# Kernel optimization log

Measured on AMD Instinct MI355X. Metric: run time of the kernel, lower is better.

## Reference

```python
import jax, jax.numpy as jnp
import numpy as np

DIM = 256
HEADS = 8
WH, WW = 8, 8
N = WH * WW
B_ = 2048
NW = 64  # num windows per image; B_ // NW = batch of 32
CPB_HIDDEN = 256


def _log_rel_index(wh, ww):
    ch = np.arange(wh)
    cw = np.arange(ww)
    coords = np.stack(np.meshgrid(ch, cw, indexing='ij'))      # (2, wh, ww)
    cf = coords.reshape(2, -1)                                  # (2, N)
    rel = cf[:, :, None] - cf[:, None, :]                       # (2, N, N)
    rel = rel.transpose(1, 2, 0).astype(np.float32)             # (N, N, 2)
    return np.sign(rel) * np.log1p(np.abs(rel))


def setup_inputs() -> dict:
    key = jax.random.key(0)
    ks = jax.random.split(key, 16)
    s = 0.02
    inp = {
        'x': jax.random.normal(ks[0], (B_, N, DIM), jnp.float32),
        'KV': jax.random.normal(ks[1], (B_, N, DIM), jnp.float32),
        'mask': jnp.zeros((NW, N, N), jnp.float32),
        # linear weights stored (in, out): y = x @ W + b
        'Wq': jax.random.normal(ks[2], (DIM, DIM), jnp.float32) * s,
        'bq': jnp.zeros((DIM,), jnp.float32),
        'Wkv': jax.random.normal(ks[3], (DIM, 2 * DIM), jnp.float32) * s,
        'bkv': jnp.zeros((2 * DIM,), jnp.float32),
        'Wp': jax.random.normal(ks[4], (DIM, DIM), jnp.float32) * s,
        'bp': jnp.zeros((DIM,), jnp.float32),
        'cpb_w1': jax.random.normal(ks[5], (2, CPB_HIDDEN), jnp.float32) * s,
        'cpb_b1': jnp.zeros((CPB_HIDDEN,), jnp.float32),
        'cpb_w2': jax.random.normal(ks[6], (CPB_HIDDEN, HEADS), jnp.float32) * s,
        'cpb_b2': jnp.zeros((HEADS,), jnp.float32),
        'tau': jnp.ones((HEADS, N, N), jnp.float32),
        'log_rel_idx': jnp.asarray(_log_rel_index(WH, WW)),  # (N, N, 2)
    }
    return inp


def reference(x, KV, mask, Wq, bq, Wkv, bkv, Wp, bp,
              cpb_w1, cpb_b1, cpb_w2, cpb_b2, tau, log_rel_idx):
    Bw, n, C = x.shape
    H = tau.shape[0]
    hd = C // H
    scale = hd ** -0.5

    q = (x @ Wq + bq).reshape(Bw, n, H, hd).transpose(0, 2, 1, 3) * scale   # (B_,H,N,hd)
    kv = (KV @ Wkv + bkv).reshape(Bw, n, 2, H, hd).transpose(2, 0, 3, 1, 4)  # (2,B_,H,N,hd)
    k, v = kv[0], kv[1]

    num = jnp.einsum('bhqd,bhkd->bhqk', q, k)
    qn = jnp.sqrt(jnp.sum(q * q, axis=-1, keepdims=True))                    # (B_,H,N,1)
    kn = jnp.sqrt(jnp.sum(k * k, axis=-1, keepdims=True))                    # (B_,H,N,1)
    denom = jnp.maximum(qn * kn.transpose(0, 1, 3, 2), 1e-6)
    attn = num / denom
    attn = attn / jnp.clip(tau[:, :n, :n], 0.01)[None]

    # continuous relative position bias MLP: (N,N,2) -> (N,N,H)
    h = jax.nn.relu(log_rel_idx[:n, :n] @ cpb_w1 + cpb_b1)
    bias = (h @ cpb_w2 + cpb_b2).transpose(2, 0, 1)                          # (H,N,N)
    attn = attn + bias[None]

    nW = mask.shape[0]
    attn = attn.reshape(Bw // nW, nW, H, n, n) + mask[None, :, None]
    attn = attn.reshape(Bw, H, n, n)
    attn = jax.nn.softmax(attn, axis=-1)

    out = jnp.einsum('bhqk,bhkd->bhqd', attn, v)
    out = out.transpose(0, 2, 1, 3).reshape(Bw, n, C)
    out = out @ Wp + bp
    return out
```

## Files before the change

### kernel.cpp

```cpp
#include <hip/hip_runtime.h>
#include <hip/hip_bf16.h>

#define NWIN 64

typedef __attribute__((ext_vector_type(8))) short v8s;
typedef __attribute__((ext_vector_type(4))) float v4f;

#define WQT_OFF   0u
#define WKVT_OFF  131072u
#define WPT_OFF   393216u
#define ITB_OFF   524288u

static __device__ __forceinline__ short f2bf(float f) {
  union { float f; unsigned int u; } v; v.f = f;
  unsigned int u = v.u;
  return (short)((u + 0x7fffu + ((u >> 16) & 1u)) >> 16);
}

static __device__ __forceinline__ int packbf(float lo, float hi) {
  __hip_bfloat162 h = __float22bfloat162_rn(float2{lo, hi});
  union { __hip_bfloat162 h; int i; } u; u.h = h; return u.i;
}

__global__ void prep_kernel(const float* __restrict__ Wq, const float* __restrict__ Wkv,
                            const float* __restrict__ Wp, const float* __restrict__ tau,
                            short* __restrict__ WqT, short* __restrict__ WkvT,
                            short* __restrict__ WpT, float2* __restrict__ itb) {
  int id = blockIdx.x * 256 + threadIdx.x;
  if (id < 65536) {
    int o = id >> 8, i = id & 255;
    WqT[id] = f2bf(Wq[i * 256 + o]);
  } else if (id < 196608) {
    int t = id - 65536; int o = t >> 8, i = t & 255;
    WkvT[t] = f2bf(Wkv[i * 512 + o]);
  } else if (id < 262144) {
    int t = id - 196608; int o = t >> 8, i = t & 255;
    WpT[t] = f2bf(Wp[i * 256 + o]);
  } else if (id < 294912) {
    int t = id - 262144;
    itb[t].x = 1.0f / fmaxf(tau[t], 0.01f);
  }
}

__global__ void cpb_kernel(const float* __restrict__ w1, const float* __restrict__ b1,
                           const float* __restrict__ w2, const float* __restrict__ b2,
                           const float* __restrict__ lri, float2* __restrict__ itb) {
  int ij = blockIdx.x * 256 + threadIdx.x;
  float l0 = lri[ij * 2], l1 = lri[ij * 2 + 1];
  float acc[8];
#pragma unroll
  for (int h = 0; h < 8; ++h) acc[h] = b2[h];
  for (int c = 0; c < 256; ++c) {
    float hv = fmaxf(l0 * w1[c] + l1 * w1[256 + c] + b1[c], 0.0f);
#pragma unroll
    for (int h = 0; h < 8; ++h) acc[h] += hv * w2[c * 8 + h];
  }
#pragma unroll
  for (int h = 0; h < 8; ++h) itb[h * 4096 + ij].y = acc[h];
}

static __device__ __forceinline__ v8s xform_tile(int p0a, int p0b, int p1a, int p1b,
                                                 int base, int mdsel) {
  int a0 = __shfl(p0a, base, 64),      b0 = __shfl(p1a, base, 64);
  int a1 = __shfl(p0b, base, 64),      b1 = __shfl(p1b, base, 64);
  int a2 = __shfl(p0a, base + 16, 64), b2 = __shfl(p1a, base + 16, 64);
  int a3 = __shfl(p0b, base + 16, 64), b3 = __shfl(p1b, base + 16, 64);
  union { v8s v; int i[4]; } r;
  r.i[0] = mdsel ? b0 : a0;
  r.i[1] = mdsel ? b1 : a1;
  r.i[2] = mdsel ? b2 : a2;
  r.i[3] = mdsel ? b3 : a3;
  return r.v;
}

__global__ __launch_bounds__(512, 4) void wattn_kernel(
    const float* __restrict__ x, const float* __restrict__ KV,
    const float* __restrict__ mask,
    const float* __restrict__ bq, const float* __restrict__ bkv,
    const float* __restrict__ bp,
    const short* __restrict__ WqT, const short* __restrict__ WkvT,
    const short* __restrict__ WpT, const float2* __restrict__ itb,
    float* __restrict__ out) {
  __shared__ short sm[33792];

  const int b = blockIdx.x;
  const int tid = threadIdx.x;
  const int w = tid >> 6;
  const int lane = tid & 63;
  const int cc = lane & 15;
  const int qd = lane >> 4;
  const int base = cc + 32 * (qd & 1);
  const int mdsel = qd >> 1;
  const v4f vzero = {0.f, 0.f, 0.f, 0.f};
  short* xs = sm;
  short* kvs = sm + 16896;

  {
    const float4* xb = (const float4*)(x + (size_t)b * 16384);
    const float4* kb = (const float4*)(KV + (size_t)b * 16384);
#pragma unroll
    for (int ii = 0; ii < 8; ++ii) {
      int i = tid + ii * 512;
      int r = i >> 6, col = (i & 63) << 2;
      float4 vx = xb[i];
      float4 vk = kb[i];
      int2 px = { packbf(vx.x, vx.y), packbf(vx.z, vx.w) };
      int2 pk = { packbf(vk.x, vk.y), packbf(vk.z, vk.w) };
      *(int2*)&xs[r * 264 + col] = px;
      *(int2*)&kvs[r * 264 + col] = pk;
    }
  }
  __syncthreads();

  v4f Dq[2][4];
#pragma unroll
  for (int md = 0; md < 2; ++md)
#pragma unroll
    for (int nt = 0; nt < 4; ++nt) Dq[md][nt] = vzero;
  {
    const short* wqb = WqT + (32 * w + cc) * 256 + qd * 8;
#pragma unroll
    for (int it = 0; it < 8; ++it) {
      v8s a0 = *(const v8s*)(wqb + it * 32);
      v8s a1 = *(const v8s*)(wqb + 16 * 256 + it * 32);
#pragma unroll
      for (int nt = 0; nt < 4; ++nt) {
        v8s bx = *(const v8s*)(xs + (nt * 16 + cc) * 264 + it * 32 + qd * 8);
        Dq[0][nt] = __builtin_amdgcn_mfma_f32_16x16x32_bf16(a0, bx, Dq[0][nt], 0, 0, 0);
        Dq[1][nt] = __builtin_amdgcn_mfma_f32_16x16x32_bf16(a1, bx, Dq[1][nt], 0, 0, 0);
      }
    }
  }
  v8s qB[4];
  {
    v4f b0 = *(const v4f*)(bq + 32 * w + qd * 4);
    v4f b1 = *(const v4f*)(bq + 32 * w + 16 + qd * 4);
#pragma unroll
    for (int nt = 0; nt < 4; ++nt) {
      float s = 0.f;
#pragma unroll
      for (int rg = 0; rg < 4; ++rg) {
        float v0 = Dq[0][nt][rg] + b0[rg];
        float v1 = Dq[1][nt][rg] + b1[rg];
        Dq[0][nt][rg] = v0; Dq[1][nt][rg] = v1;
        s += v0 * v0 + v1 * v1;
      }
      s += __shfl_xor(s, 16); s += __shfl_xor(s, 32);
      float inv = rsqrtf(s + 1e-24f);
      int p00 = packbf(Dq[0][nt][0] * inv, Dq[0][nt][1] * inv);
      int p01 = packbf(Dq[0][nt][2] * inv, Dq[0][nt][3] * inv);
      int p10 = packbf(Dq[1][nt][0] * inv, Dq[1][nt][1] * inv);
      int p11 = packbf(Dq[1][nt][2] * inv, Dq[1][nt][3] * inv);
      qB[nt] = xform_tile(p00, p01, p10, p11, base, mdsel);
    }
  }

  v4f Dk[2][4], Dv[4][2];
#pragma unroll
  for (int nt = 0; nt < 4; ++nt) {
    Dk[0][nt] = vzero; Dk[1][nt] = vzero;
    Dv[nt][0] = vzero; Dv[nt][1] = vzero;
  }
  {
    const short* wkb = WkvT + (32 * w + cc) * 256 + qd * 8;
    const short* wvb = WkvT + (256 + 32 * w + cc) * 256 + qd * 8;
#pragma unroll
    for (int it = 0; it < 8; ++it) {
      v8s ak0 = *(const v8s*)(wkb + it * 32);
      v8s ak1 = *(const v8s*)(wkb + 16 * 256 + it * 32);
      v8s bv0 = *(const v8s*)(wvb + it * 32);
      v8s bv1 = *(const v8s*)(wvb + 16 * 256 + it * 32);
#pragma unroll
      for (int nt = 0; nt < 4; ++nt) {
        v8s kf = *(const v8s*)(kvs + (nt * 16 + cc) * 264 + it * 32 + qd * 8);
        Dk[0][nt] = __builtin_amdgcn_mfma_f32_16x16x32_bf16(ak0, kf, Dk[0][nt], 0, 0, 0);
        Dk[1][nt] = __builtin_amdgcn_mfma_f32_16x16x32_bf16(ak1, kf, Dk[1][nt], 0, 0, 0);
        Dv[nt][0] = __builtin_amdgcn_mfma_f32_16x16x32_bf16(kf, bv0, Dv[nt][0], 0, 0, 0);
        Dv[nt][1] = __builtin_amdgcn_mfma_f32_16x16x32_bf16(kf, bv1, Dv[nt][1], 0, 0, 0);
      }
    }
  }
  v8s kA[4];
  {
    v4f b0 = *(const v4f*)(bkv + 32 * w + qd * 4);
    v4f b1 = *(const v4f*)(bkv + 32 * w + 16 + qd * 4);
#pragma unroll
    for (int nt = 0; nt < 4; ++nt) {
      float s = 0.f;
#pragma unroll
      for (int rg = 0; rg < 4; ++rg) {
        float v0 = Dk[0][nt][rg] + b0[rg];
        float v1 = Dk[1][nt][rg] + b1[rg];
        Dk[0][nt][rg] = v0; Dk[1][nt][rg] = v1;
        s += v0 * v0 + v1 * v1;
      }
      s += __shfl_xor(s, 16); s += __shfl_xor(s, 32);
      float inv = rsqrtf(s + 1e-24f);
      int p00 = packbf(Dk[0][nt][0] * inv, Dk[0][nt][1] * inv);
      int p01 = packbf(Dk[0][nt][2] * inv, Dk[0][nt][3] * inv);
      int p10 = packbf(Dk[1][nt][0] * inv, Dk[1][nt][1] * inv);
      int p11 = packbf(Dk[1][nt][2] * inv, Dk[1][nt][3] * inv);
      kA[nt] = xform_tile(p00, p01, p10, p11, base, mdsel);
    }
  }
  v8s av[2][2];
  {
    float bv0 = bkv[256 + 32 * w + cc];
    float bv1 = bkv[256 + 32 * w + 16 + cc];
    int Pv[4][2][2];
#pragma unroll
    for (int vt = 0; vt < 4; ++vt) {
      Pv[vt][0][0] = packbf(Dv[vt][0][0] + bv0, Dv[vt][0][1] + bv0);
      Pv[vt][0][1] = packbf(Dv[vt][0][2] + bv0, Dv[vt][0][3] + bv0);
      Pv[vt][1][0] = packbf(Dv[vt][1][0] + bv1, Dv[vt][1][1] + bv1);
      Pv[vt][1][1] = packbf(Dv[vt][1][2] + bv1, Dv[vt][1][3] + bv1);
    }
#pragma unroll
    for (int md = 0; md < 2; ++md)
#pragma unroll
      for (int kc = 0; kc < 2; ++kc)
        av[md][kc] = xform_tile(Pv[2 * kc][md][0], Pv[2 * kc][md][1],
                                Pv[2 * kc + 1][md][0], Pv[2 * kc + 1][md][1], base, mdsel);
  }

  v4f Sv[4][4];
#pragma unroll
  for (int jt = 0; jt < 4; ++jt)
#pragma unroll
    for (int it = 0; it < 4; ++it)
      Sv[jt][it] = __builtin_amdgcn_mfma_f32_16x16x32_bf16(kA[jt], qB[it], vzero, 0, 0, 0);

  {
    const float4* itb4 = (const float4*)(itb + (size_t)w * 4096);
    const float4* mw4 = (const float4*)(mask + (size_t)(b & (NWIN - 1)) * 4096);
#pragma unroll
    for (int it = 0; it < 4; ++it) {
      int i = it * 16 + cc;
#pragma unroll
      for (int jt = 0; jt < 4; ++jt) {
        int e = i * 64 + jt * 16 + qd * 4;
        float4 A = itb4[e >> 1];
        float4 B = itb4[(e >> 1) + 1];
        float4 M = mw4[e >> 2];
        Sv[jt][it][0] = Sv[jt][it][0] * A.x + A.y + M.x;
        Sv[jt][it][1] = Sv[jt][it][1] * A.z + A.w + M.y;
        Sv[jt][it][2] = Sv[jt][it][2] * B.x + B.y + M.z;
        Sv[jt][it][3] = Sv[jt][it][3] * B.z + B.w + M.w;
      }
      float mx = -3.4e38f;
#pragma unroll
      for (int jt = 0; jt < 4; ++jt)
#pragma unroll
        for (int rg = 0; rg < 4; ++rg) mx = fmaxf(mx, Sv[jt][it][rg]);
      mx = fmaxf(mx, __shfl_xor(mx, 16)); mx = fmaxf(mx, __shfl_xor(mx, 32));
      float sum = 0.f;
#pragma unroll
      for (int jt = 0; jt < 4; ++jt)
#pragma unroll
        for (int rg = 0; rg < 4; ++rg) {
          float ev = __expf(Sv[jt][it][rg] - mx);
          Sv[jt][it][rg] = ev;
          sum += ev;
        }
      sum += __shfl_xor(sum, 16); sum += __shfl_xor(sum, 32);
      float rs = 1.0f / sum;
#pragma unroll
      for (int jt = 0; jt < 4; ++jt)
#pragma unroll
        for (int rg = 0; rg < 4; ++rg) Sv[jt][it][rg] *= rs;
    }
  }

  v4f Do[2][4];
  {
#pragma unroll
    for (int it = 0; it < 4; ++it) {
      int pp[4][2];
#pragma unroll
      for (int jt = 0; jt < 4; ++jt) {
        pp[jt][0] = packbf(Sv[jt][it][0], Sv[jt][it][1]);
        pp[jt][1] = packbf(Sv[jt][it][2], Sv[jt][it][3]);
      }
      v8s pB0 = xform_tile(pp[0][0], pp[0][1], pp[1][0], pp[1][1], base, mdsel);
      v8s pB1 = xform_tile(pp[2][0], pp[2][1], pp[3][0], pp[3][1], base, mdsel);
#pragma unroll
      for (int md = 0; md < 2; ++md) {
        v4f t = __builtin_amdgcn_mfma_f32_16x16x32_bf16(av[md][0], pB0, vzero, 0, 0, 0);
        Do[md][it] = __builtin_amdgcn_mfma_f32_16x16x32_bf16(av[md][1], pB1, t, 0, 0, 0);
      }
    }
  }

  __syncthreads();
#pragma unroll
  for (int md = 0; md < 2; ++md)
#pragma unroll
    for (int it = 0; it < 4; ++it) {
      int addr = (it * 16 + cc) * 264 + 32 * w + md * 16 + qd * 4;
      *(int*)&sm[addr] = packbf(Do[md][it][0], Do[md][it][1]);
      *(int*)&sm[addr + 2] = packbf(Do[md][it][2], Do[md][it][3]);
    }
  __syncthreads();

  v4f pa[4][2];
#pragma unroll
  for (int mt = 0; mt < 4; ++mt) { pa[mt][0] = vzero; pa[mt][1] = vzero; }
  {
    const short* wpb = WpT + (32 * w + cc) * 256 + qd * 8;
#pragma unroll
    for (int it = 0; it < 8; ++it) {
      v8s b0 = *(const v8s*)(wpb + it * 32);
      v8s b1 = *(const v8s*)(wpb + 16 * 256 + it * 32);
#pragma unroll
      for (int mt = 0; mt < 4; ++mt) {
        v8s a = *(const v8s*)(sm + (mt * 16 + cc) * 264 + it * 32 + qd * 8);
        pa[mt][0] = __builtin_amdgcn_mfma_f32_16x16x32_bf16(a, b0, pa[mt][0], 0, 0, 0);
        pa[mt][1] = __builtin_amdgcn_mfma_f32_16x16x32_bf16(a, b1, pa[mt][1], 0, 0, 0);
      }
    }
  }
  {
    float b0 = bp[32 * w + cc], b1 = bp[32 * w + 16 + cc];
    float* ob = out + (size_t)b * 16384;
#pragma unroll
    for (int mt = 0; mt < 4; ++mt)
#pragma unroll
      for (int rg = 0; rg < 4; ++rg) {
        int row = mt * 16 + qd * 4 + rg;
        ob[row * 256 + 32 * w + cc] = pa[mt][0][rg] + b0;
        ob[row * 256 + 32 * w + 16 + cc] = pa[mt][1][rg] + b1;
      }
  }
}

extern "C" void kernel_launch(void* const* d_in, const int* in_sizes, int n_in,
                              void* d_out, int out_size, void* d_ws, size_t ws_size,
                              hipStream_t stream) {
  const float* x    = (const float*)d_in[0];
  const float* KV   = (const float*)d_in[1];
  const float* mask = (const float*)d_in[2];
  const float* Wq   = (const float*)d_in[3];
  const float* bq   = (const float*)d_in[4];
  const float* Wkv  = (const float*)d_in[5];
  const float* bkv  = (const float*)d_in[6];
  const float* Wp   = (const float*)d_in[7];
  const float* bp   = (const float*)d_in[8];
  const float* cw1  = (const float*)d_in[9];
  const float* cb1  = (const float*)d_in[10];
  const float* cw2  = (const float*)d_in[11];
  const float* cb2  = (const float*)d_in[12];
  const float* tau  = (const float*)d_in[13];
  const float* lri  = (const float*)d_in[14];

  unsigned char* ws = (unsigned char*)d_ws;
  short* WqT   = (short*)(ws + WQT_OFF);
  short* WkvT  = (short*)(ws + WKVT_OFF);
  short* WpT   = (short*)(ws + WPT_OFF);
  float2* itb  = (float2*)(ws + ITB_OFF);

  prep_kernel<<<1152, 256, 0, stream>>>(Wq, Wkv, Wp, tau, WqT, WkvT, WpT, itb);
  cpb_kernel<<<16, 256, 0, stream>>>(cw1, cb1, cw2, cb2, lri, itb);
  wattn_kernel<<<2048, 512, 0, stream>>>(x, KV, mask, bq, bkv, bp,
                                         WqT, WkvT, WpT, itb, (float*)d_out);
}
```

Before: 562.0 us.

## Batch global loads, prefetch Wq, stage P through swizzled LDS, add setprio

The input conversion loop now issues four float4 loads for x and KV before packing, and the first half of Wq fragments is loaded into registers before the barrier so global latency overlaps the LDS fill. The bias and mask loads are batched ahead of their FMAs. The softmax probabilities are now repacked through a per-wave XOR-swizzled LDS scratch area in the freed kvs buffer instead of register shuffles (xform_tile), with the barrier moved earlier. s_setprio brackets around the MFMA sections give those waves issue priority. The cost is more registers held live and extra LDS traffic for the P transpose.

```diff
diff --git a/kernel.cpp b/kernel.cpp
--- a/kernel.cpp
+++ b/kernel.cpp
@@ -99,16 +99,31 @@
     const float4* xb = (const float4*)(x + (size_t)b * 16384);
     const float4* kb = (const float4*)(KV + (size_t)b * 16384);
 #pragma unroll
-    for (int ii = 0; ii < 8; ++ii) {
-      int i = tid + ii * 512;
-      int r = i >> 6, col = (i & 63) << 2;
-      float4 vx = xb[i];
-      float4 vk = kb[i];
-      int2 px = { packbf(vx.x, vx.y), packbf(vx.z, vx.w) };
-      int2 pk = { packbf(vk.x, vk.y), packbf(vk.z, vk.w) };
-      *(int2*)&xs[r * 264 + col] = px;
-      *(int2*)&kvs[r * 264 + col] = pk;
-    }
+    for (int half = 0; half < 2; ++half) {
+      float4 vx[4], vk[4];
+#pragma unroll
+      for (int ii = 0; ii < 4; ++ii) {
+        int i = tid + (half * 4 + ii) * 512;
+        vx[ii] = xb[i];
+        vk[ii] = kb[i];
+      }
+#pragma unroll
+      for (int ii = 0; ii < 4; ++ii) {
+        int i = tid + (half * 4 + ii) * 512;
+        int r = i >> 6, col = (i & 63) << 2;
+        int2 px = { packbf(vx[ii].x, vx[ii].y), packbf(vx[ii].z, vx[ii].w) };
+        int2 pk = { packbf(vk[ii].x, vk[ii].y), packbf(vk[ii].z, vk[ii].w) };
+        *(int2*)&xs[r * 264 + col] = px;
+        *(int2*)&kvs[r * 264 + col] = pk;
+      }
+    }
+  }
+  const short* wqb = WqT + (32 * w + cc) * 256 + qd * 8;
+  v8s wq0[4], wq1[4];
+#pragma unroll
+  for (int it = 0; it < 4; ++it) {
+    wq0[it] = *(const v8s*)(wqb + it * 32);
+    wq1[it] = *(const v8s*)(wqb + 16 * 256 + it * 32);
   }
   __syncthreads();
 
@@ -118,9 +133,17 @@
 #pragma unroll
     for (int nt = 0; nt < 4; ++nt) Dq[md][nt] = vzero;
   {
-    const short* wqb = WqT + (32 * w + cc) * 256 + qd * 8;
-#pragma unroll
-    for (int it = 0; it < 8; ++it) {
+#pragma unroll
+    for (int it = 0; it < 4; ++it) {
+#pragma unroll
+      for (int nt = 0; nt < 4; ++nt) {
+        v8s bx = *(const v8s*)(xs + (nt * 16 + cc) * 264 + it * 32 + qd * 8);
+        Dq[0][nt] = __builtin_amdgcn_mfma_f32_16x16x32_bf16(wq0[it], bx, Dq[0][nt], 0, 0, 0);
+        Dq[1][nt] = __builtin_amdgcn_mfma_f32_16x16x32_bf16(wq1[it], bx, Dq[1][nt], 0, 0, 0);
+      }
+    }
+#pragma unroll
+    for (int it = 4; it < 8; ++it) {
       v8s a0 = *(const v8s*)(wqb + it * 32);
       v8s a1 = *(const v8s*)(wqb + 16 * 256 + it * 32);
 #pragma unroll
@@ -224,11 +247,13 @@
   }
 
   v4f Sv[4][4];
+  __builtin_amdgcn_s_setprio(1);
 #pragma unroll
   for (int jt = 0; jt < 4; ++jt)
 #pragma unroll
     for (int it = 0; it < 4; ++it)
       Sv[jt][it] = __builtin_amdgcn_mfma_f32_16x16x32_bf16(kA[jt], qB[it], vzero, 0, 0, 0);
+  __builtin_amdgcn_s_setprio(0);
 
   {
     const float4* itb4 = (const float4*)(itb + (size_t)w * 4096);
@@ -236,16 +261,25 @@
 #pragma unroll
     for (int it = 0; it < 4; ++it) {
       int i = it * 16 + cc;
-#pragma unroll
-      for (int jt = 0; jt < 4; ++jt) {
-        int e = i * 64 + jt * 16 + qd * 4;
-        float4 A = itb4[e >> 1];
-        float4 B = itb4[(e >> 1) + 1];
-        float4 M = mw4[e >> 2];
-        Sv[jt][it][0] = Sv[jt][it][0] * A.x + A.y + M.x;
-        Sv[jt][it][1] = Sv[jt][it][1] * A.z + A.w + M.y;
-        Sv[jt][it][2] = Sv[jt][it][2] * B.x + B.y + M.z;
-        Sv[jt][it][3] = Sv[jt][it][3] * B.z + B.w + M.w;
+      float4 A[4], Bv[4], Mv[4];
+#pragma unroll
+      for (int jh = 0; jh < 2; ++jh) {
+#pragma unroll
+        for (int j2 = 0; j2 < 2; ++j2) {
+          int jt = jh * 2 + j2;
+          int e = i * 64 + jt * 16 + qd * 4;
+          A[jt] = itb4[e >> 1];
+          Bv[jt] = itb4[(e >> 1) + 1];
+          Mv[jt] = mw4[e >> 2];
+        }
+#pragma unroll
+        for (int j2 = 0; j2 < 2; ++j2) {
+          int jt = jh * 2 + j2;
+          Sv[jt][it][0] = Sv[jt][it][0] * A[jt].x + A[jt].y + Mv[jt].x;
+          Sv[jt][it][1] = Sv[jt][it][1] * A[jt].z + A[jt].w + Mv[jt].y;
+          Sv[jt][it][2] = Sv[jt][it][2] * Bv[jt].x + Bv[jt].y + Mv[jt].z;
+          Sv[jt][it][3] = Sv[jt][it][3] * Bv[jt].z + Bv[jt].w + Mv[jt].w;
+        }
       }
       float mx = -3.4e38f;
 #pragma unroll
@@ -271,27 +305,35 @@
     }
   }
 
+  __syncthreads();
   v4f Do[2][4];
   {
+    char* psw = (char*)kvs + w * 4096;
 #pragma unroll
     for (int it = 0; it < 4; ++it) {
-      int pp[4][2];
+      char* ps = psw + (it & 1) * 2048;
 #pragma unroll
       for (int jt = 0; jt < 4; ++jt) {
-        pp[jt][0] = packbf(Sv[jt][it][0], Sv[jt][it][1]);
-        pp[jt][1] = packbf(Sv[jt][it][2], Sv[jt][it][3]);
-      }
-      v8s pB0 = xform_tile(pp[0][0], pp[0][1], pp[1][0], pp[1][1], base, mdsel);
-      v8s pB1 = xform_tile(pp[2][0], pp[2][1], pp[3][0], pp[3][1], base, mdsel);
+        int2 pr;
+        pr.x = packbf(Sv[jt][it][0], Sv[jt][it][1]);
+        pr.y = packbf(Sv[jt][it][2], Sv[jt][it][3]);
+        int byte = (cc * 128 + jt * 32 + qd * 8) ^ ((cc & 7) << 4);
+        *(int2*)(ps + byte) = pr;
+      }
+      int rb0 = (cc * 128 + qd * 16) ^ ((cc & 7) << 4);
+      int rb1 = (cc * 128 + 64 + qd * 16) ^ ((cc & 7) << 4);
+      v8s pB0 = *(const v8s*)(ps + rb0);
+      v8s pB1 = *(const v8s*)(ps + rb1);
+      __builtin_amdgcn_s_setprio(1);
 #pragma unroll
       for (int md = 0; md < 2; ++md) {
         v4f t = __builtin_amdgcn_mfma_f32_16x16x32_bf16(av[md][0], pB0, vzero, 0, 0, 0);
         Do[md][it] = __builtin_amdgcn_mfma_f32_16x16x32_bf16(av[md][1], pB1, t, 0, 0, 0);
       }
-    }
-  }
-
-  __syncthreads();
+      __builtin_amdgcn_s_setprio(0);
+    }
+  }
+
 #pragma unroll
   for (int md = 0; md < 2; ++md)
 #pragma unroll
```

New measurement: 550.1 us. 1.02x faster.
